# Kernel tuning notes

Hardware: AMD Instinct MI355X
Metric: run time of the kernel (lower is better)

## Reference

```python
import jax, jax.numpy as jnp
import numpy as np
from functools import partial

REGION_NUM = 5
ALPHA = 0.02


def _otsu(u8, N):
    """Per-batch Otsu threshold. u8: (B, N) int32 in [0,255] -> (B,) int32.
    Matches cv2.THRESH_OTSU: argmax over t of between-class variance with
    class0 = bins <= t, binarization is pixel > t."""
    B = u8.shape[0]
    hist = jnp.zeros((B, 256), jnp.float32).at[jnp.arange(B)[:, None], u8].add(1.0)
    p = hist / N
    bins = jnp.arange(256, dtype=jnp.float32)
    w0 = jnp.cumsum(p, axis=1)                 # class-0 mass up to bin t
    mu = jnp.cumsum(p * bins, axis=1)          # class-0 first moment
    mu_t = mu[:, -1:]                          # total mean
    sigma_b = (mu_t * w0 - mu) ** 2 / (w0 * (1.0 - w0) + 1e-12)
    return jnp.argmax(sigma_b, axis=1)         # first max, like OpenCV


def _cc_label(mask):
    """8-connected components via iterative min-label propagation.
    mask: (H, W) bool -> (H, W) int32 labels; 0 = background, components get
    the (min flat index + 1) of their pixels as a unique id in 1..N."""
    H, W = mask.shape
    N = H * W
    BIG = jnp.int32(N + 1)
    idx = jnp.arange(1, N + 1, dtype=jnp.int32).reshape(H, W)
    lab0 = jnp.where(mask, idx, BIG)

    def step(l):
        p = jnp.pad(l, 1, constant_values=N + 1)
        nb = jnp.stack([p[i:i + H, j:j + W] for i in range(3) for j in range(3)])
        return jnp.where(mask, jnp.min(nb, axis=0), BIG)

    def cond(s):
        _, changed, it = s
        return changed & (it < N)

    def body(s):
        l, _, it = s
        nl = step(l)
        return (nl, jnp.any(nl != l), it + 1)

    lab, _, _ = jax.lax.while_loop(cond, body, (lab0, jnp.bool_(True), jnp.int32(0)))
    return jnp.where(mask, lab, 0)


def _forward(z, query_z):
    B, N, D = z.shape
    H = W = int(round(N ** 0.5))
    K = REGION_NUM - 1

    # similarity score + per-batch min-max normalization
    sim = jnp.einsum('bd,bnd->bn', query_z[:, 0], z) / (D ** 0.5)   # (B, N)
    smin = jnp.min(sim, axis=1, keepdims=True)
    smax = jnp.max(sim, axis=1, keepdims=True)
    sal = (sim - smin) / (smax - smin + 1e-6)
    sal = jax.lax.stop_gradient(sal)  # torch detaches before the numpy/cv2 pipeline

    # uint8 quantization (truncation, like .astype(np.uint8)) + Otsu binarization
    u8 = jnp.clip(jnp.floor(sal * 255.0), 0, 255).astype(jnp.int32)
    t = _otsu(u8, N)                              # (B,)
    binary = u8 > t[:, None]                      # (B, N) bool

    # connected components per image
    labels = jax.vmap(_cc_label)(binary.reshape(B, H, W)).reshape(B, N)  # 0..N

    # per-component area and mean saliency
    seg = partial(jax.ops.segment_sum, num_segments=N + 1)
    area = jax.vmap(seg)(jnp.ones((B, N), jnp.float32), labels)   # (B, N+1)
    ssum = jax.vmap(seg)(sal, labels)                              # (B, N+1)
    mean = ssum / jnp.maximum(area, 1.0)

    # keep components with area >= ALPHA*N (label 0 = non-mask excluded)
    valid = (area >= ALPHA * N) & (jnp.arange(N + 1) > 0)
    cand = jnp.where(valid, mean, -jnp.inf)

    # top-(region_num-1) components by mean saliency
    top_s, top_l = jax.lax.top_k(cand, K)         # (B, K)
    sel = jnp.isfinite(top_s)                     # (B, K)
    region = (labels[:, None, :] == top_l[:, :, None]) & sel[:, :, None]  # (B, K, N)
    bg = ~jnp.any(region, axis=1)                 # background = complement of union
    return jnp.concatenate([region, bg[:, None, :]], axis=1).astype(z.dtype)


def setup_inputs() -> dict:
    key = jax.random.key(0)
    k1, k2 = jax.random.split(key)
    B, N, D = 64, 1024, 768
    return {
        'z': jax.random.normal(k1, (B, N, D), dtype=jnp.float32),
        'query_z': jax.random.normal(k2, (B, 1, D), dtype=jnp.float32),
    }


def reference(z, query_z):
    return _forward(z, query_z)
```

## Files before the change

### kernel.cpp

```cpp
#include <hip/hip_runtime.h>
#include <stdint.h>

#define NB   64
#define NPIX 1024
#define DIM  768
#define KTOP 4

__global__ __launch_bounds__(256) void sgatt_sim(const float* __restrict__ z,
                                                 const float* __restrict__ q,
                                                 float* __restrict__ sim) {
    const int b    = blockIdx.y;
    const int lane = threadIdx.x & 63;
    const int wave = threadIdx.x >> 6;
    const float4* qv = reinterpret_cast<const float4*>(q + (size_t)b * DIM);
    const float4 q0 = qv[lane], q1 = qv[lane + 64], q2 = qv[lane + 128];
    const float rt = sqrtf((float)DIM);
#pragma unroll
    for (int r = 0; r < 4; ++r) {
        const int row = blockIdx.x * 16 + wave * 4 + r;
        const float4* zv =
            reinterpret_cast<const float4*>(z + (size_t)(b * NPIX + row) * DIM);
        const float4 z0 = zv[lane], z1 = zv[lane + 64], z2 = zv[lane + 128];
        double acc = (double)z0.x * q0.x + (double)z0.y * q0.y +
                     (double)z0.z * q0.z + (double)z0.w * q0.w;
        acc += (double)z1.x * q1.x + (double)z1.y * q1.y +
               (double)z1.z * q1.z + (double)z1.w * q1.w;
        acc += (double)z2.x * q2.x + (double)z2.y * q2.y +
               (double)z2.z * q2.z + (double)z2.w * q2.w;
#pragma unroll
        for (int o = 32; o > 0; o >>= 1) acc += __shfl_xor(acc, o);
        if (lane == 0) sim[b * NPIX + row] = (float)acc / rt;
    }
}

__device__ inline int uf_find(volatile int* p, int x) {
    int px = p[x];
    while (px != x) { x = px; px = p[x]; }
    return x;
}

__device__ inline void uf_union(volatile int* p, int a, int b) {
    while (true) {
        a = uf_find(p, a);
        b = uf_find(p, b);
        if (a == b) return;
        const int hi = a > b ? a : b;
        const int lo = a ^ b ^ hi;
        const int old = atomicCAS((int*)&p[hi], hi, lo);
        if (old == hi) return;
        a = old; b = lo;
    }
}

__global__ __launch_bounds__(256) void sgatt_region(const float* __restrict__ sim,
                                                    float* __restrict__ out) {
    const int b    = blockIdx.x;
    const int t    = threadIdx.x;
    const int lane = t & 63;
    const int wid  = t >> 6;

    __shared__ float s_sal[NPIX];
    __shared__ int   s_par[NPIX];
    __shared__ unsigned int s_mbits[NPIX / 32];
    __shared__ int   s_hist[256];
    __shared__ float s_wA[4], s_wB[4];
    __shared__ float s_avv[4];
    __shared__ int   s_avi[4];
    __shared__ int   s_area[NPIX + 1];
    __shared__ float s_ssum[NPIX + 1];
    __shared__ unsigned long long s_part[4];
    __shared__ unsigned long long s_win;
    __shared__ float s_smin, s_smax;
    __shared__ int   s_thr;
    __shared__ int   s_top[KTOP];

    const float4 sv4 =
        reinterpret_cast<const float4*>(sim + (size_t)b * NPIX)[t];
    const float svj[4] = {sv4.x, sv4.y, sv4.z, sv4.w};
    float mn = fminf(fminf(svj[0], svj[1]), fminf(svj[2], svj[3]));
    float mx = fmaxf(fmaxf(svj[0], svj[1]), fmaxf(svj[2], svj[3]));
#pragma unroll
    for (int o = 32; o > 0; o >>= 1) {
        mn = fminf(mn, __shfl_xor(mn, o));
        mx = fmaxf(mx, __shfl_xor(mx, o));
    }
    if (lane == 0) { s_wA[wid] = mn; s_wB[wid] = mx; }
    s_hist[t] = 0;
    if (t < NPIX / 32) s_mbits[t] = 0u;
#pragma unroll
    for (int j = 0; j < 4; ++j) { s_area[4*t + j] = 0; s_ssum[4*t + j] = 0.0f; }
    if (t == 0) { s_area[NPIX] = 0; s_ssum[NPIX] = 0.0f; }
    __syncthreads();
    if (t == 0) {
        float a = s_wA[0], c = s_wB[0];
        for (int w = 1; w < 4; ++w) { a = fminf(a, s_wA[w]); c = fmaxf(c, s_wB[w]); }
        s_smin = a; s_smax = c;
    }
    __syncthreads();

    const float smin = s_smin;
    const float den0 = __fadd_rn(__fsub_rn(s_smax, smin), 1e-6f);
    int u8j[4];
#pragma unroll
    for (int j = 0; j < 4; ++j) {
        const float sal = __fdiv_rn(__fsub_rn(svj[j], smin), den0);
        s_sal[4*t + j] = sal;
        int u = (int)floorf(__fmul_rn(sal, 255.0f));
        u8j[j] = min(max(u, 0), 255);
        atomicAdd(&s_hist[u8j[j]], 1);
    }
    __syncthreads();

    {
        const float p = __fmul_rn((float)s_hist[t], 1.0f / 1024.0f);
        float w0 = p;
        float mu = __fmul_rn(p, (float)t);
#pragma unroll
        for (int o = 1; o < 64; o <<= 1) {
            const float aw = __shfl_up(w0, o);
            const float am = __shfl_up(mu, o);
            if (lane >= o) { w0 = __fadd_rn(w0, aw); mu = __fadd_rn(mu, am); }
        }
        if (lane == 63) { s_wA[wid] = w0; s_wB[wid] = mu; }
        __syncthreads();
        float mut = 0.0f;
        for (int w = 0; w < 4; ++w) mut = __fadd_rn(mut, s_wB[w]);
        for (int w = 0; w < wid; ++w) {
            w0 = __fadd_rn(w0, s_wA[w]);
            mu = __fadd_rn(mu, s_wB[w]);
        }
        const float num = __fsub_rn(__fmul_rn(mut, w0), mu);
        const float dn  = __fadd_rn(__fmul_rn(w0, __fsub_rn(1.0f, w0)), 1e-12f);
        float v  = __fdiv_rn(__fmul_rn(num, num), dn);
        int   idx = t;
#pragma unroll
        for (int o = 32; o > 0; o >>= 1) {
            const float v2 = __shfl_xor(v, o);
            const int   i2 = __shfl_xor(idx, o);
            if (v2 > v || (v2 == v && i2 < idx)) { v = v2; idx = i2; }
        }
        if (lane == 0) { s_avv[wid] = v; s_avi[wid] = idx; }
    }
    __syncthreads();
    if (t == 0) {
        float bv = s_avv[0]; int bi = s_avi[0];
        for (int w = 1; w < 4; ++w)
            if (s_avv[w] > bv || (s_avv[w] == bv && s_avi[w] < bi)) {
                bv = s_avv[w]; bi = s_avi[w];
            }
        s_thr = bi;
    }
    __syncthreads();
    const int thr = s_thr;

    int mj[4];
#pragma unroll
    for (int j = 0; j < 4; ++j) {
        const int px = 4*t + j;
        mj[j] = (u8j[j] > thr) ? 1 : 0;
        s_par[px] = px;
        if (mj[j]) atomicOr(&s_mbits[px >> 5], 1u << (px & 31));
    }
    __syncthreads();

#pragma unroll
    for (int j = 0; j < 4; ++j) {
        if (!mj[j]) continue;
        const int px = 4*t + j;
        const int r = px >> 5, c = px & 31;
#define ONMASK(p) ((s_mbits[(p) >> 5] >> ((p) & 31)) & 1u)
        if (c > 0 && ONMASK(px - 1))  uf_union(s_par, px, px - 1);
        if (r > 0) {
            if (c > 0 && ONMASK(px - 33)) uf_union(s_par, px, px - 33);
            if (ONMASK(px - 32))          uf_union(s_par, px, px - 32);
            if (c < 31 && ONMASK(px - 31)) uf_union(s_par, px, px - 31);
        }
#undef ONMASK
    }
    __syncthreads();

    int labj[4];
#pragma unroll
    for (int j = 0; j < 4; ++j) {
        const int px = 4*t + j;
        labj[j] = mj[j] ? (uf_find(s_par, px) + 1) : 0;
        if (mj[j]) {
            atomicAdd(&s_area[labj[j]], 1);
            atomicAdd(&s_ssum[labj[j]], s_sal[px]);
        }
    }
    __syncthreads();

    unsigned long long key[4];
#pragma unroll
    for (int j = 0; j < 4; ++j) {
        const int L = 4*t + j + 1;
        const int a = s_area[L];
        key[j] = 0ull;
        if (a >= 21) {
            const float mean = __fdiv_rn(s_ssum[L], (float)a);
            key[j] = ((unsigned long long)__float_as_uint(mean) << 32) |
                     (unsigned long long)(0xFFFFFFFFu - (unsigned)L);
        }
    }
    for (int k = 0; k < KTOP; ++k) {
        unsigned long long v =
            max(max(key[0], key[1]), max(key[2], key[3]));
#pragma unroll
        for (int o = 32; o > 0; o >>= 1) {
            const unsigned long long w = __shfl_xor(v, o);
            if (w > v) v = w;
        }
        if (lane == 0) s_part[wid] = v;
        __syncthreads();
        if (t == 0) {
            unsigned long long bb = s_part[0];
            for (int w2 = 1; w2 < 4; ++w2)
                if (s_part[w2] > bb) bb = s_part[w2];
            s_win = bb;
            s_top[k] = (bb != 0ull)
                           ? (int)(0xFFFFFFFFu - (unsigned)(bb & 0xFFFFFFFFull))
                           : -1;
        }
        __syncthreads();
        const unsigned long long win = s_win;
#pragma unroll
        for (int j = 0; j < 4; ++j)
            if (key[j] == win && win != 0ull) key[j] = 0ull;
    }

    float* ob = out + (size_t)b * 5 * NPIX;
    int anyr[4] = {0, 0, 0, 0};
#pragma unroll
    for (int k = 0; k < KTOP; ++k) {
        const int tl = s_top[k];
        float4 o;
        float* op = reinterpret_cast<float*>(&o);
#pragma unroll
        for (int j = 0; j < 4; ++j) {
            const int match = (tl >= 0 && labj[j] == tl) ? 1 : 0;
            anyr[j] |= match;
            op[j] = (float)match;
        }
        reinterpret_cast<float4*>(ob + (size_t)k * NPIX)[t] = o;
    }
    {
        float4 o;
        float* op = reinterpret_cast<float*>(&o);
#pragma unroll
        for (int j = 0; j < 4; ++j) op[j] = anyr[j] ? 0.0f : 1.0f;
        reinterpret_cast<float4*>(ob + (size_t)KTOP * NPIX)[t] = o;
    }
}

extern "C" void kernel_launch(void* const* d_in, const int* in_sizes, int n_in,
                              void* d_out, int out_size, void* d_ws, size_t ws_size,
                              hipStream_t stream) {
    const float* z = (const float*)d_in[0];
    const float* q = (const float*)d_in[1];
    float* out = (float*)d_out;
    float* sim = (float*)d_ws;

    dim3 g1(NPIX / 16, NB);
    sgatt_sim<<<g1, 256, 0, stream>>>(z, q, sim);
    sgatt_region<<<NB, 256, 0, stream>>>(sim, out);
}
```

Measured before the change: 60.38 us.

## Fuse similarity and region kernels via last-block-done atomic counter

```diff
diff --git a/kernel.cpp b/kernel.cpp
--- a/kernel.cpp
+++ b/kernel.cpp
@@ -6,36 +6,14 @@
 #define DIM  768
 #define KTOP 4
 
-__global__ __launch_bounds__(256) void sgatt_sim(const float* __restrict__ z,
-                                                 const float* __restrict__ q,
-                                                 float* __restrict__ sim) {
-    const int b    = blockIdx.y;
-    const int lane = threadIdx.x & 63;
-    const int wave = threadIdx.x >> 6;
-    const float4* qv = reinterpret_cast<const float4*>(q + (size_t)b * DIM);
-    const float4 q0 = qv[lane], q1 = qv[lane + 64], q2 = qv[lane + 128];
-    const float rt = sqrtf((float)DIM);
-#pragma unroll
-    for (int r = 0; r < 4; ++r) {
-        const int row = blockIdx.x * 16 + wave * 4 + r;
-        const float4* zv =
-            reinterpret_cast<const float4*>(z + (size_t)(b * NPIX + row) * DIM);
-        const float4 z0 = zv[lane], z1 = zv[lane + 64], z2 = zv[lane + 128];
-        double acc = (double)z0.x * q0.x + (double)z0.y * q0.y +
-                     (double)z0.z * q0.z + (double)z0.w * q0.w;
-        acc += (double)z1.x * q1.x + (double)z1.y * q1.y +
-               (double)z1.z * q1.z + (double)z1.w * q1.w;
-        acc += (double)z2.x * q2.x + (double)z2.y * q2.y +
-               (double)z2.z * q2.z + (double)z2.w * q2.w;
-#pragma unroll
-        for (int o = 32; o > 0; o >>= 1) acc += __shfl_xor(acc, o);
-        if (lane == 0) sim[b * NPIX + row] = (float)acc / rt;
-    }
-}
-
 __device__ inline int uf_find(volatile int* p, int x) {
     int px = p[x];
-    while (px != x) { x = px; px = p[x]; }
+    while (px != x) {
+        const int g = p[px];
+        if (g != px) p[x] = g;
+        x = g;
+        px = p[x];
+    }
     return x;
 }
 
@@ -52,12 +30,46 @@
     }
 }
 
-__global__ __launch_bounds__(256) void sgatt_region(const float* __restrict__ sim,
-                                                    float* __restrict__ out) {
-    const int b    = blockIdx.x;
+__global__ __launch_bounds__(256) void sgatt_fused(const float* __restrict__ z,
+                                                   const float* __restrict__ q,
+                                                   float* __restrict__ sim,
+                                                   int* __restrict__ cnt,
+                                                   float* __restrict__ out) {
+    const int b    = blockIdx.y;
     const int t    = threadIdx.x;
     const int lane = t & 63;
     const int wid  = t >> 6;
+
+    {
+        const float4* qv = reinterpret_cast<const float4*>(q + (size_t)b * DIM);
+        const float4 q0 = qv[lane], q1 = qv[lane + 64], q2 = qv[lane + 128];
+        const float rt = sqrtf((float)DIM);
+#pragma unroll
+        for (int r = 0; r < 4; ++r) {
+            const int row = blockIdx.x * 16 + wid * 4 + r;
+            const float4* zv =
+                reinterpret_cast<const float4*>(z + (size_t)(b * NPIX + row) * DIM);
+            const float4 z0 = zv[lane], z1 = zv[lane + 64], z2 = zv[lane + 128];
+            double acc = (double)z0.x * q0.x + (double)z0.y * q0.y +
+                         (double)z0.z * q0.z + (double)z0.w * q0.w;
+            acc += (double)z1.x * q1.x + (double)z1.y * q1.y +
+                   (double)z1.z * q1.z + (double)z1.w * q1.w;
+            acc += (double)z2.x * q2.x + (double)z2.y * q2.y +
+                   (double)z2.z * q2.z + (double)z2.w * q2.w;
+#pragma unroll
+            for (int o = 32; o > 0; o >>= 1) acc += __shfl_xor(acc, o);
+            if (lane == 0) sim[b * NPIX + row] = (float)acc / rt;
+        }
+    }
+    __syncthreads();
+    __shared__ int s_lastblk;
+    if (t == 0) {
+        __threadfence();
+        s_lastblk = (atomicAdd(&cnt[b], 1) == NB - 1) ? 1 : 0;
+    }
+    __syncthreads();
+    if (!s_lastblk) return;
+    __threadfence();
 
     __shared__ float s_sal[NPIX];
     __shared__ int   s_par[NPIX];
@@ -260,8 +272,10 @@
     const float* q = (const float*)d_in[1];
     float* out = (float*)d_out;
     float* sim = (float*)d_ws;
-
-    dim3 g1(NPIX / 16, NB);
-    sgatt_sim<<<g1, 256, 0, stream>>>(z, q, sim);
-    sgatt_region<<<NB, 256, 0, stream>>>(sim, out);
-}
+    int*   cnt = (int*)((char*)d_ws + (size_t)NB * NPIX * 4);
+
+    hipMemsetAsync(cnt, 0, NB * sizeof(int), stream);
+
+    dim3 g(NPIX / 16, NB);
+    sgatt_fused<<<g, 256, 0, stream>>>(z, q, sim, cnt, out);
+}
```

Measured after the change: 240.6 us. 3.99x slower.
